# Optimization experiments

Measured on AMD Instinct MI355X. Metric: run time of the kernel, lower is better.

The kernel has to match this reference:

```python
import jax, jax.numpy as jnp
import numpy as np

# Config (matches init_kwargs defaults): V=25 joints, C=16 -> D=400, heads=2,
# ffn=64*25=1600, window L=9, stride=1, postnorm, gelu, dropout ignored (eval).
N, C, T, V = 16, 16, 300, 25
D = C * V          # 400
H = 2              # nhead
FF = 64 * V        # 1600
L = 9              # trans_length
MAX_LEN = 301


def _layernorm(x, g, b, eps=1e-5):
    mu = jnp.mean(x, axis=-1, keepdims=True)
    var = jnp.mean(jnp.square(x - mu), axis=-1, keepdims=True)
    return (x - mu) * jax.lax.rsqrt(var + eps) * g + b


def setup_inputs() -> dict:
    key = jax.random.key(0)
    ks = jax.random.split(key, 12)
    s = 0.02
    return {
        "x": jax.random.normal(ks[0], (N, C, T, V), jnp.float32),
        "pe": jax.random.normal(ks[1], (1, MAX_LEN, D), jnp.float32) * s,
        "w_in": jax.random.normal(ks[2], (3 * D, D), jnp.float32) * s,
        "b_in": jnp.zeros((3 * D,), jnp.float32),
        "w_out": jax.random.normal(ks[3], (D, D), jnp.float32) * s,
        "b_out": jnp.zeros((D,), jnp.float32),
        "w1": jax.random.normal(ks[4], (FF, D), jnp.float32) * s,
        "b1": jnp.zeros((FF,), jnp.float32),
        "w2": jax.random.normal(ks[5], (D, FF), jnp.float32) * s,
        "b2": jnp.zeros((D,), jnp.float32),
        "ln1_g": jnp.ones((D,), jnp.float32),
        "ln1_b": jnp.zeros((D,), jnp.float32),
        "ln2_g": jnp.ones((D,), jnp.float32),
        "ln2_b": jnp.zeros((D,), jnp.float32),
    }


def _encoder_layer(h, w_in, b_in, w_out, b_out, w1, b1, w2, b2,
                   ln1_g, ln1_b, ln2_g, ln2_b):
    # h: [B, L, D]; post-norm TransformerEncoderLayer (torch default)
    B, Lw, Dm = h.shape
    dh = Dm // H
    qkv = h @ w_in.T + b_in                             # [B,L,3D]
    q, k, v = jnp.split(qkv, 3, axis=-1)
    def heads(t):
        return t.reshape(B, Lw, H, dh).transpose(0, 2, 1, 3)  # [B,H,L,dh]
    q, k, v = heads(q), heads(k), heads(v)
    scores = jnp.einsum('bhqd,bhkd->bhqk', q, k) / np.float32(np.sqrt(dh))
    att = jax.nn.softmax(scores, axis=-1)
    o = jnp.einsum('bhqk,bhkd->bhqd', att, v)
    o = o.transpose(0, 2, 1, 3).reshape(B, Lw, Dm) @ w_out.T + b_out
    h = _layernorm(h + o, ln1_g, ln1_b)
    ff = jax.nn.gelu(h @ w1.T + b1, approximate=False) @ w2.T + b2
    return _layernorm(h + ff, ln2_g, ln2_b)


def reference(x, pe, w_in, b_in, w_out, b_out, w1, b1, w2, b2,
              ln1_g, ln1_b, ln2_g, ln2_b):
    n, c, t, v = x.shape
    d = c * v
    # [N,C,T,V] -> [N,T,V,C] -> [N,T,D]  (flatten order is (V,C), as in torch view)
    xs = x.transpose(0, 2, 3, 1).reshape(n, t, d)
    xs = xs + pe[:, :t, :]
    W = t - L                                            # number of windows (stride=1)
    win = jnp.arange(W)
    idx = win[:, None] + jnp.arange(L)[None, :]          # [W,L] gather indices
    xw = xs[:, idx, :].reshape(n * W, L, d)              # batched windows
    out = _encoder_layer(xw, w_in, b_in, w_out, b_out, w1, b1, w2, b2,
                         ln1_g, ln1_b, ln2_g, ln2_b)
    out = out.reshape(n, W * L, d)
    # window i writes into rows i//2 : i//2 + L and results are summed
    pos = ((win // 2)[:, None] + jnp.arange(L)[None, :]).reshape(-1)  # [W*L]
    xt = jnp.zeros((n, t, d), xs.dtype).at[:, pos, :].add(out)
    # [N,T,D] -> [N,T,V,C] -> [N,C,T,V]
    return xt.reshape(n, t, v, c).transpose(0, 3, 1, 2)
```

## Files before the change

kernel.cpp:

```cpp
#include <hip/hip_runtime.h>
#include <cstdint>
#include <cstddef>

#define N_    16
#define C_    16
#define T_    300
#define V_    25
#define D_    400
#define H_    2
#define DH_   200
#define FF_   1600
#define L_    9
#define W_    291
#define NW_   (N_*W_)
#define NT_   (N_*T_)

#define KP_   416
#define SD_   400
#define SQKV_ 1200
#define SFF_  1600

#define WIN_OFF   0u
#define WOUT_OFF  1064960u
#define W1_OFF    1490944u
#define W2_OFF    2875392u
#define XS_OFF    4513792u
#define QKV_OFF   8404992u
#define ACC_OFF   20078592u
#define HEAD_END  27758592u

#define WAIT_VM4   0xF74
#define WAIT_VM0   0xF70

using u16 = unsigned short;
using u32 = unsigned int;
using frag  = __attribute__((ext_vector_type(8))) short;
using f32x4 = __attribute__((ext_vector_type(4))) float;

__device__ __forceinline__ float bf2f(u16 u){
  return __uint_as_float(((u32)u) << 16);
}
__device__ __forceinline__ u16 f2bf(float f){
  return (u16)((__float_as_uint(f) + 0x8000u) >> 16);
}
__device__ __forceinline__ float gelu_f(float v){
  float v2  = v * v;
  float u   = v * (0.7978845608f + 0.03567740814f * v2);
  float u2  = u * u;
  float num = u * (27.f + u2);
  float den = 27.f + 9.f * u2;
  float th  = num * __builtin_amdgcn_rcpf(den);
  th = fminf(fmaxf(th, -1.f), 1.f);
  return 0.5f * v * (1.f + th);
}
__device__ __forceinline__ void unpack8(uint4 v, float* o){
  o[0] = bf2f((u16)(v.x & 0xffffu)); o[1] = bf2f((u16)(v.x >> 16));
  o[2] = bf2f((u16)(v.y & 0xffffu)); o[3] = bf2f((u16)(v.y >> 16));
  o[4] = bf2f((u16)(v.z & 0xffffu)); o[5] = bf2f((u16)(v.z >> 16));
  o[6] = bf2f((u16)(v.w & 0xffffu)); o[7] = bf2f((u16)(v.w >> 16));
}

__device__ __forceinline__ void convw_body(const float* src, u16* dst,
                                           int dN, int dK, int sN, int sK, int idx){
  if (idx >= dN * dK) return;
  int n = idx / dK, k = idx % dK;
  dst[idx] = (n < sN && k < sK) ? f2bf(src[(size_t)n * sK + k]) : (u16)0;
}

#define PREP_GRID 23816
__global__ __launch_bounds__(256) void prep_kernel(const float* __restrict__ x,
                                                   const float* __restrict__ pe,
                                                   const float* __restrict__ w_in,
                                                   const float* __restrict__ w_out,
                                                   const float* __restrict__ w1,
                                                   const float* __restrict__ w2,
                                                   u16* __restrict__ xs,
                                                   u16* __restrict__ w_in_b,
                                                   u16* __restrict__ w_out_b,
                                                   u16* __restrict__ w1_b,
                                                   u16* __restrict__ w2_b,
                                                   float* __restrict__ acc){
  int b = blockIdx.x;
  int tid = threadIdx.x;
  if (b < 7500){
    int idx = b * 256 + tid;
    if (idx < NT_ * D_) acc[idx] = 0.f;
  } else if (b < 15000){
    int idx = (b - 7500) * 256 + tid;
    if (idx < NT_ * D_){
      int d  = idx % D_;
      int nt = idx / D_;
      int t  = nt % T_;
      int n  = nt / T_;
      float val = x[(((size_t)(n*C_ + (d & 15)))*T_ + t)*V_ + (d >> 4)] + pe[t*D_ + d];
      xs[idx] = f2bf(val);
    }
  } else if (b < 17080){
    convw_body(w_in,  w_in_b,  1280, KP_, 1200, D_,  (b - 15000) * 256 + tid);
  } else if (b < 17912){
    convw_body(w_out, w_out_b,  512, KP_,  400, D_,  (b - 17080) * 256 + tid);
  } else if (b < 20616){
    convw_body(w1,    w1_b,   1664, KP_, 1600, D_,  (b - 17912) * 256 + tid);
  } else {
    convw_body(w2,    w2_b,    512, SFF_, 400, FF_, (b - 20616) * 256 + tid);
  }
}

template<int ACT>
__global__ __launch_bounds__(256) void gemm_mfma(const u16* __restrict__ A, int lda,
                                                 const u16* __restrict__ B, int ldb,
                                                 const float* __restrict__ bias,
                                                 u16* __restrict__ C, int ldc,
                                                 int Nn, int KPd,
                                                 int gx, int gy){
  __shared__ u16 smem[24576];
  int id = blockIdx.x;
  int c  = id & 7, t = id >> 3;
  int bx = t % gx;
  int by = (t / gx) * 8 + c;
  if (by >= gy) return;
  const int m0 = by * 128, n0 = bx * 128;

  const int tid  = threadIdx.x;
  const int lane = tid & 63;
  const int wv   = tid >> 6;
  const int quad = lane >> 4, l16 = lane & 15;
  const int wm   = wv & 1,   wn  = wv >> 1;

  const int rl   = lane >> 2;
  const int sseg = (lane & 3) ^ ((lane >> 3) & 3);
  const u16* Ag = A + (size_t)(m0 + wv*32 + rl) * lda + sseg*8;
  const u16* Bg = B + (size_t)(n0 + wv*32 + rl) * ldb + sseg*8;

  f32x4 acc[4][4] = {};
  const int sa = quad ^ ((l16 >> 1) & 3);

  auto stage = [&](int buf, int kt){
    u16* Ad = &smem[buf*4096 + (wv*32)*32];
    u16* Bd = &smem[12288 + buf*4096 + (wv*32)*32];
    #pragma unroll
    for (int h = 0; h < 2; ++h){
      __builtin_amdgcn_global_load_lds(
          (const __attribute__((address_space(1))) void*)(Ag + kt + (size_t)(16*h)*lda),
          (__attribute__((address_space(3))) void*)(Ad + h*16*32), 16, 0, 0);
      __builtin_amdgcn_global_load_lds(
          (const __attribute__((address_space(1))) void*)(Bg + kt + (size_t)(16*h)*ldb),
          (__attribute__((address_space(3))) void*)(Bd + h*16*32), 16, 0, 0);
    }
  };

  const int nit = KPd >> 5;
  stage(0, 0);
  stage(1, 32);
  int nb = 2;
  for (int it = 0; it < nit; ++it){
    if (it < nit - 1) __builtin_amdgcn_s_waitcnt(WAIT_VM4);
    else              __builtin_amdgcn_s_waitcnt(WAIT_VM0);
    __builtin_amdgcn_s_barrier();
    if (it + 2 < nit){
      stage(nb, (it + 2) << 5);
      nb = (nb == 2) ? 0 : nb + 1;
    }
    const int buf = it % 3;
    const u16* Ar = &smem[buf*4096];
    const u16* Br = &smem[12288 + buf*4096];
    frag af[4], bfr[4];
    #pragma unroll
    for (int i = 0; i < 4; ++i){
      af[i]  = *(const frag*)(&Ar[(wm*64 + i*16 + l16)*32 + sa*8]);
      bfr[i] = *(const frag*)(&Br[(wn*64 + i*16 + l16)*32 + sa*8]);
    }
    #pragma unroll
    for (int i = 0; i < 4; ++i)
      #pragma unroll
      for (int j = 0; j < 4; ++j)
        acc[i][j] = __builtin_amdgcn_mfma_f32_16x16x32_bf16(af[i], bfr[j], acc[i][j], 0, 0, 0);
  }

  __builtin_amdgcn_s_barrier();

  u16* ep = &smem[wv * 4608];
  #pragma unroll
  for (int j = 0; j < 4; ++j){
    int n = n0 + wn*64 + j*16 + l16;
    float bj = (n < Nn) ? bias[n] : 0.f;
    #pragma unroll
    for (int i = 0; i < 4; ++i){
      #pragma unroll
      for (int r = 0; r < 4; ++r){
        float v = acc[i][j][r] + bj;
        if (ACT) v = gelu_f(v);
        ep[(i*16 + quad*4 + r)*72 + j*16 + l16] = f2bf(v);
      }
    }
  }
  #pragma unroll
  for (int p = 0; p < 8; ++p){
    int row = p*8 + (lane >> 3);
    int seg = lane & 7;
    int nc  = n0 + wn*64 + seg*8;
    if (nc < Nn){
      uint4 v = *(const uint4*)(&ep[row*72 + seg*8]);
      *(uint4*)(C + (size_t)(m0 + wm*64 + row)*ldc + nc) = v;
    }
  }
}

__global__ __launch_bounds__(256) void attn_kernel(const u16* __restrict__ qkv,
                                                   u16* __restrict__ o,
                                                   int g0){
  __shared__ float sq[L_ * 1200];
  __shared__ float sc[H_ * L_ * L_];
  __shared__ float att[H_ * L_ * L_];
  const int g = g0 + blockIdx.x;
  const int n = g / W_, w = g % W_;
  const int tid = threadIdx.x;

  for (int i = tid; i < L_ * 150; i += 256){
    int l = i / 150, ck = i % 150;
    uint4 v = *(const uint4*)(qkv + ((size_t)(n*T_ + w + l)) * SQKV_ + ck*8);
    unpack8(v, &sq[l*1200 + ck*8]);
  }
  __syncthreads();

  if (tid < H_ * L_ * L_){
    int h = tid / (L_*L_), rem = tid % (L_*L_), qi = rem / L_, ki = rem % L_;
    const float* qp = &sq[qi*1200 + h*DH_];
    const float* kp = &sq[ki*1200 + D_ + h*DH_];
    float s = 0.f;
    for (int dd = 0; dd < DH_; ++dd) s += qp[dd] * kp[dd];
    sc[tid] = s * 0.07071067811865475f;
  }
  __syncthreads();

  if (tid < H_ * L_){
    int base = tid * L_;
    float mx = -1e30f;
    for (int j = 0; j < L_; ++j) mx = fmaxf(mx, sc[base + j]);
    float sum = 0.f;
    for (int j = 0; j < L_; ++j){ float e = __expf(sc[base + j] - mx); att[base + j] = e; sum += e; }
    float inv = 1.f / sum;
    for (int j = 0; j < L_; ++j) att[base + j] *= inv;
  }
  __syncthreads();

  for (int i = tid; i < L_ * D_; i += 256){
    int l = i / D_, d = i % D_;
    int h = d / DH_;
    float a = 0.f;
    #pragma unroll
    for (int ki = 0; ki < L_; ++ki)
      a += att[h*(L_*L_) + l*L_ + ki] * sq[ki*1200 + 2*D_ + d];
    o[((size_t)blockIdx.x * L_ + l) * SD_ + d] = f2bf(a);
  }
}

__global__ __launch_bounds__(256) void ln1_kernel(const u16* __restrict__ y,
                                                  const float* __restrict__ gam,
                                                  const float* __restrict__ bet,
                                                  u16* __restrict__ out,
                                                  const u16* __restrict__ xs,
                                                  int g0){
  const int wv = threadIdx.x >> 6, lane = threadIdx.x & 63;
  const int r = blockIdx.x * 4 + wv;
  const int g = g0 + r / L_, l = r % L_;
  const int n = g / W_, w = g % W_;
  const u16* arow = xs + ((size_t)(n*T_ + w + l)) * SD_;
  const u16* brow = y + (size_t)r * SD_;

  const bool act = lane < 50;
  float v[8];
  float s = 0.f, s2 = 0.f;
  if (act){
    float a8[8], b8[8];
    unpack8(*(const uint4*)(arow + lane*8), a8);
    unpack8(*(const uint4*)(brow + lane*8), b8);
    #pragma unroll
    for (int i = 0; i < 8; ++i){ v[i] = a8[i] + b8[i]; s += v[i]; s2 += v[i]*v[i]; }
  } else {
    #pragma unroll
    for (int i = 0; i < 8; ++i) v[i] = 0.f;
  }
  #pragma unroll
  for (int off = 32; off; off >>= 1){
    s  += __shfl_xor(s,  off);
    s2 += __shfl_xor(s2, off);
  }
  float mean = s * (1.f / D_);
  float rstd = rsqrtf(s2 * (1.f / D_) - mean*mean + 1e-5f);
  if (act){
    float4 ga = *(const float4*)(gam + lane*8);
    float4 gb = *(const float4*)(gam + lane*8 + 4);
    float4 ba = *(const float4*)(bet + lane*8);
    float4 bb = *(const float4*)(bet + lane*8 + 4);
    float gg[8] = {ga.x,ga.y,ga.z,ga.w, gb.x,gb.y,gb.z,gb.w};
    float bb8[8]= {ba.x,ba.y,ba.z,ba.w, bb.x,bb.y,bb.z,bb.w};
    u32 o4[4];
    #pragma unroll
    for (int i = 0; i < 4; ++i){
      u16 lo = f2bf((v[2*i]   - mean) * rstd * gg[2*i]   + bb8[2*i]);
      u16 hi = f2bf((v[2*i+1] - mean) * rstd * gg[2*i+1] + bb8[2*i+1]);
      o4[i] = (u32)lo | ((u32)hi << 16);
    }
    *(uint4*)(out + (size_t)r * SD_ + lane*8) = make_uint4(o4[0],o4[1],o4[2],o4[3]);
  }
}

__global__ __launch_bounds__(256) void ln2_scatter_kernel(const u16* __restrict__ h,
                                                          const u16* __restrict__ y,
                                                          const float* __restrict__ gam,
                                                          const float* __restrict__ bet,
                                                          float* __restrict__ acc,
                                                          int g0){
  __shared__ float buf[4][400];
  const int wv = threadIdx.x >> 6, lane = threadIdx.x & 63;
  const int tid = threadIdx.x;
  const int r0 = blockIdx.x * 4;
  {
    const int r = r0 + wv;
    const u16* arow = h + (size_t)r * SD_;
    const u16* brow = y + (size_t)r * SD_;
    const bool act = lane < 50;
    float v[8];
    float s = 0.f, s2 = 0.f;
    if (act){
      float a8[8], b8[8];
      unpack8(*(const uint4*)(arow + lane*8), a8);
      unpack8(*(const uint4*)(brow + lane*8), b8);
      #pragma unroll
      for (int i = 0; i < 8; ++i){ v[i] = a8[i] + b8[i]; s += v[i]; s2 += v[i]*v[i]; }
    } else {
      #pragma unroll
      for (int i = 0; i < 8; ++i) v[i] = 0.f;
    }
    #pragma unroll
    for (int off = 32; off; off >>= 1){
      s  += __shfl_xor(s,  off);
      s2 += __shfl_xor(s2, off);
    }
    float mean = s * (1.f / D_);
    float rstd = rsqrtf(s2 * (1.f / D_) - mean*mean + 1e-5f);
    if (act){
      float4 ga = *(const float4*)(gam + lane*8);
      float4 gb = *(const float4*)(gam + lane*8 + 4);
      float4 ba = *(const float4*)(bet + lane*8);
      float4 bb = *(const float4*)(bet + lane*8 + 4);
      float gg[8] = {ga.x,ga.y,ga.z,ga.w, gb.x,gb.y,gb.z,gb.w};
      float bb8[8]= {ba.x,ba.y,ba.z,ba.w, bb.x,bb.y,bb.z,bb.w};
      #pragma unroll
      for (int i = 0; i < 8; ++i)
        buf[wv][lane*8 + i] = (v[i] - mean) * rstd * gg[i] + bb8[i];
    }
  }
  __syncthreads();
  #pragma unroll
  for (int rr = 0; rr < 4; ++rr){
    int r = r0 + rr;
    int g = g0 + r / L_, l = r % L_;
    int n = g / W_, w = g % W_;
    size_t base = ((size_t)(n*T_ + (w >> 1) + l)) * D_;
    atomicAdd(acc + base + tid, buf[rr][tid]);
    if (tid + 256 < D_) atomicAdd(acc + base + tid + 256, buf[rr][tid + 256]);
  }
}

__global__ __launch_bounds__(256) void final_kernel(const float* __restrict__ acc,
                                                    float* __restrict__ dout){
  int idx = blockIdx.x * 256 + threadIdx.x;
  if (idx >= NT_ * D_) return;
  int d  = idx % D_;
  int nt = idx / D_;
  int t  = nt % T_;
  int n  = nt / T_;
  dout[(((size_t)(n*C_ + (d & 15)))*T_ + t)*V_ + (d >> 4)] = acc[idx];
}

extern "C" void kernel_launch(void* const* d_in, const int* in_sizes, int n_in,
                              void* d_out, int out_size, void* d_ws, size_t ws_size,
                              hipStream_t stream){
  (void)in_sizes; (void)n_in; (void)out_size;
  const float* x     = (const float*)d_in[0];
  const float* pe    = (const float*)d_in[1];
  const float* w_in  = (const float*)d_in[2];
  const float* b_in  = (const float*)d_in[3];
  const float* w_out = (const float*)d_in[4];
  const float* b_out = (const float*)d_in[5];
  const float* w1    = (const float*)d_in[6];
  const float* b1    = (const float*)d_in[7];
  const float* w2    = (const float*)d_in[8];
  const float* b2    = (const float*)d_in[9];
  const float* ln1g  = (const float*)d_in[10];
  const float* ln1b  = (const float*)d_in[11];
  const float* ln2g  = (const float*)d_in[12];
  const float* ln2b  = (const float*)d_in[13];

  int nch = 3;
  {
    size_t need1 = (size_t)HEAD_END + (size_t)41984 * 5600;
    size_t need2 = (size_t)HEAD_END + (size_t)20992 * 5600;
    if (ws_size >= need1 + (1u<<20)) nch = 1;
    else if (ws_size >= need2 + (1u<<20)) nch = 2;
  }
  const int CW  = NW_ / nch;
  const int RC  = CW * L_;
  const int RCP = ((RC + 127) / 128) * 128;

  char* ws = (char*)d_ws;
  u16*   w_in_b  = (u16*)(ws + WIN_OFF);
  u16*   w_out_b = (u16*)(ws + WOUT_OFF);
  u16*   w1_b    = (u16*)(ws + W1_OFF);
  u16*   w2_b    = (u16*)(ws + W2_OFF);
  u16*   xs      = (u16*)(ws + XS_OFF);
  u16*   qkv     = (u16*)(ws + QKV_OFF);
  float* acc     = (float*)(ws + ACC_OFF);
  u16*   o_c     = (u16*)(ws + HEAD_END);
  u16*   y_c     = o_c + (size_t)RCP * SD_;
  u16*   h_c     = y_c + (size_t)RCP * SD_;
  u16*   ffc     = h_c + (size_t)RCP * SD_;

  prep_kernel<<<PREP_GRID, 256, 0, stream>>>(x, pe, w_in, w_out, w1, w2,
                                             xs, w_in_b, w_out_b, w1_b, w2_b, acc);

  {
    int gx = 10, gy = (NT_ + 127)/128, gy8 = (gy + 7) & ~7;
    gemm_mfma<0><<<gx*gy8, 256, 0, stream>>>(
        xs, SD_, w_in_b, KP_, b_in, qkv, SQKV_, 1200, KP_, gx, gy);
  }

  const int gyc = RCP/128, gyc8 = (gyc + 7) & ~7;

  for (int g0 = 0; g0 < NW_; g0 += CW){
    attn_kernel<<<CW, 256, 0, stream>>>(qkv, o_c, g0);

    gemm_mfma<0><<<4*gyc8, 256, 0, stream>>>(
        o_c, SD_, w_out_b, KP_, b_out, y_c, SD_, D_, KP_, 4, gyc);

    ln1_kernel<<<RC/4, 256, 0, stream>>>(y_c, ln1g, ln1b, h_c, xs, g0);

    gemm_mfma<1><<<13*gyc8, 256, 0, stream>>>(
        h_c, SD_, w1_b, KP_, b1, ffc, SFF_, FF_, KP_, 13, gyc);

    gemm_mfma<0><<<4*gyc8, 256, 0, stream>>>(
        ffc, SFF_, w2_b, SFF_, b2, y_c, SD_, D_, SFF_, 4, gyc);

    ln2_scatter_kernel<<<RC/4, 256, 0, stream>>>(h_c, y_c, ln2g, ln2b, acc, g0);
  }

  final_kernel<<<(NT_*D_ + 255)/256, 256, 0, stream>>>(acc, (float*)d_out);
}
```

Baseline: 441.4 us.

## Replace direct global-to-LDS loads with register-staged double-buffered GEMM pipeline

The GEMM main loop now loads A/B tiles into registers with ordinary vector loads and writes them to shared memory, instead of using global_load_lds into a triple buffer. The loop is unrolled by two over a double LDS buffer, with two register sets keeping loads two iterations ahead. Shared memory drops from 24576 to 18432 u16 and launch bounds request 3 blocks per CU, aiming for higher occupancy. The trade-off is extra registers and explicit LDS stores, which may cause spills under the tighter register budget. It also relies on hand-placed waitcnt values matching the compiler's instruction order.

```diff
diff --git a/kernel.cpp b/kernel.cpp
--- a/kernel.cpp
+++ b/kernel.cpp
@@ -31,6 +31,7 @@
 
 #define WAIT_VM4   0xF74
 #define WAIT_VM0   0xF70
+#define WAIT_LGKM0 0xC07F
 
 using u16 = unsigned short;
 using u32 = unsigned int;
@@ -107,13 +108,13 @@
 }
 
 template<int ACT>
-__global__ __launch_bounds__(256) void gemm_mfma(const u16* __restrict__ A, int lda,
-                                                 const u16* __restrict__ B, int ldb,
-                                                 const float* __restrict__ bias,
-                                                 u16* __restrict__ C, int ldc,
-                                                 int Nn, int KPd,
-                                                 int gx, int gy){
-  __shared__ u16 smem[24576];
+__global__ __launch_bounds__(256, 3) void gemm_mfma(const u16* __restrict__ A, int lda,
+                                                    const u16* __restrict__ B, int ldb,
+                                                    const float* __restrict__ bias,
+                                                    u16* __restrict__ C, int ldc,
+                                                    int Nn, int KPd,
+                                                    int gx, int gy){
+  __shared__ u16 smem[18432];
   int id = blockIdx.x;
   int c  = id & 7, t = id >> 3;
   int bx = t % gx;
@@ -131,39 +132,42 @@
   const int sseg = (lane & 3) ^ ((lane >> 3) & 3);
   const u16* Ag = A + (size_t)(m0 + wv*32 + rl) * lda + sseg*8;
   const u16* Bg = B + (size_t)(n0 + wv*32 + rl) * ldb + sseg*8;
+  const size_t a16 = (size_t)16 * lda, b16 = (size_t)16 * ldb;
+  const int wofs = (wv*32 + rl)*32 + (lane & 3)*8;
+
+  uint4 ra0h0, ra0h1, rb0h0, rb0h1;
+  uint4 ra1h0, ra1h1, rb1h0, rb1h1;
 
   f32x4 acc[4][4] = {};
   const int sa = quad ^ ((l16 >> 1) & 3);
 
-  auto stage = [&](int buf, int kt){
-    u16* Ad = &smem[buf*4096 + (wv*32)*32];
-    u16* Bd = &smem[12288 + buf*4096 + (wv*32)*32];
-    #pragma unroll
-    for (int h = 0; h < 2; ++h){
-      __builtin_amdgcn_global_load_lds(
-          (const __attribute__((address_space(1))) void*)(Ag + kt + (size_t)(16*h)*lda),
-          (__attribute__((address_space(3))) void*)(Ad + h*16*32), 16, 0, 0);
-      __builtin_amdgcn_global_load_lds(
-          (const __attribute__((address_space(1))) void*)(Bg + kt + (size_t)(16*h)*ldb),
-          (__attribute__((address_space(3))) void*)(Bd + h*16*32), 16, 0, 0);
-    }
+  auto load0 = [&](int kt){
+    ra0h0 = *(const uint4*)(Ag + kt);
+    ra0h1 = *(const uint4*)(Ag + kt + a16);
+    rb0h0 = *(const uint4*)(Bg + kt);
+    rb0h1 = *(const uint4*)(Bg + kt + b16);
   };
-
-  const int nit = KPd >> 5;
-  stage(0, 0);
-  stage(1, 32);
-  int nb = 2;
-  for (int it = 0; it < nit; ++it){
-    if (it < nit - 1) __builtin_amdgcn_s_waitcnt(WAIT_VM4);
-    else              __builtin_amdgcn_s_waitcnt(WAIT_VM0);
-    __builtin_amdgcn_s_barrier();
-    if (it + 2 < nit){
-      stage(nb, (it + 2) << 5);
-      nb = (nb == 2) ? 0 : nb + 1;
-    }
-    const int buf = it % 3;
+  auto load1 = [&](int kt){
+    ra1h0 = *(const uint4*)(Ag + kt);
+    ra1h1 = *(const uint4*)(Ag + kt + a16);
+    rb1h0 = *(const uint4*)(Bg + kt);
+    rb1h1 = *(const uint4*)(Bg + kt + b16);
+  };
+  auto wstage0 = [&](int buf){
+    *(uint4*)(&smem[buf*4096 + wofs])              = ra0h0;
+    *(uint4*)(&smem[buf*4096 + 512 + wofs])        = ra0h1;
+    *(uint4*)(&smem[8192 + buf*4096 + wofs])       = rb0h0;
+    *(uint4*)(&smem[8192 + buf*4096 + 512 + wofs]) = rb0h1;
+  };
+  auto wstage1 = [&](int buf){
+    *(uint4*)(&smem[buf*4096 + wofs])              = ra1h0;
+    *(uint4*)(&smem[buf*4096 + 512 + wofs])        = ra1h1;
+    *(uint4*)(&smem[8192 + buf*4096 + wofs])       = rb1h0;
+    *(uint4*)(&smem[8192 + buf*4096 + 512 + wofs]) = rb1h1;
+  };
+  auto compute = [&](int buf){
     const u16* Ar = &smem[buf*4096];
-    const u16* Br = &smem[12288 + buf*4096];
+    const u16* Br = &smem[8192 + buf*4096];
     frag af[4], bfr[4];
     #pragma unroll
     for (int i = 0; i < 4; ++i){
@@ -175,9 +179,40 @@
       #pragma unroll
       for (int j = 0; j < 4; ++j)
         acc[i][j] = __builtin_amdgcn_mfma_f32_16x16x32_bf16(af[i], bfr[j], acc[i][j], 0, 0, 0);
-  }
-
+  };
+
+  const int nit = KPd >> 5;
+  load0(0);
+  if (nit > 1) load1(32);
+  if (nit > 1) __builtin_amdgcn_s_waitcnt(WAIT_VM4);
+  else         __builtin_amdgcn_s_waitcnt(WAIT_VM0);
+  wstage0(0);
+  if (nit > 2) load0(64);
+  __builtin_amdgcn_s_waitcnt(WAIT_LGKM0);
   __builtin_amdgcn_s_barrier();
+
+  for (int it = 0; it < nit; it += 2){
+    if (it + 1 < nit){
+      if (it + 2 < nit) __builtin_amdgcn_s_waitcnt(WAIT_VM4);
+      else              __builtin_amdgcn_s_waitcnt(WAIT_VM0);
+      wstage1(1);
+      if (it + 3 < nit) load1((it + 3) << 5);
+    }
+    compute(0);
+    __builtin_amdgcn_s_waitcnt(WAIT_LGKM0);
+    __builtin_amdgcn_s_barrier();
+    if (it + 1 < nit){
+      if (it + 2 < nit){
+        if (it + 3 < nit) __builtin_amdgcn_s_waitcnt(WAIT_VM4);
+        else              __builtin_amdgcn_s_waitcnt(WAIT_VM0);
+        wstage0(0);
+        if (it + 4 < nit) load0((it + 4) << 5);
+      }
+      compute(1);
+      __builtin_amdgcn_s_waitcnt(WAIT_LGKM0);
+      __builtin_amdgcn_s_barrier();
+    }
+  }
 
   u16* ep = &smem[wv * 4608];
   #pragma unroll
```

Result: slower. 452.9 us (+2.6%).
